# Kernel tuning notes

Measured on AMD Instinct MI355X. Metric: run time of the kernel, lower is better.

The kernel has to match this reference:

```python
import jax, jax.numpy as jnp
import numpy as np

TOP_K = 8
NUM_GROUPS = 8


def setup_inputs() -> dict:
    key = jax.random.key(0)
    ks = jax.random.split(key, 6)
    T_B, T_S, H, I, E, G = 1, 2048, 2048, 768, 32, NUM_GROUPS
    hidden_states = jax.random.normal(ks[0], (T_B, T_S, H), dtype=jnp.float32)
    gate_weight = jax.random.normal(ks[1], (E, H), dtype=jnp.float32) * 0.02
    gate_up_proj = jax.random.normal(ks[2], (E, 2 * I, H), dtype=jnp.float32) * 0.02
    down_proj = jax.random.normal(ks[3], (E, H, I), dtype=jnp.float32) * 0.02
    merge_groups = jax.random.randint(ks[4], (E,), 0, G, dtype=jnp.int64)
    # ensure every group id appears at least once so dominant experts are well-defined
    merge_groups = merge_groups.at[:G].set(jnp.arange(G, dtype=jnp.int64))
    dominant_experts = jax.random.randint(ks[5], (G,), 0, E, dtype=jnp.int64)
    return {
        "hidden_states": hidden_states,
        "gate_weight": gate_weight,
        "gate_up_proj": gate_up_proj,
        "down_proj": down_proj,
        "merge_groups": merge_groups,
        "dominant_experts": dominant_experts,
    }


def reference(hidden_states, gate_weight, gate_up_proj, down_proj, merge_groups, dominant_experts):
    B, S, H = hidden_states.shape
    G = dominant_experts.shape[0]
    x = hidden_states.reshape(-1, H)  # [T, H]

    # Router: softmax over all experts, then top-k of the probabilities (as in source)
    logits = jnp.einsum("th,eh->te", x, gate_weight)
    probs = jax.nn.softmax(logits.astype(jnp.float32), axis=-1).astype(logits.dtype)
    top_val, top_idx = jax.lax.top_k(probs, TOP_K)  # [T, K]
    top_val = top_val / jnp.sum(top_val, axis=-1, keepdims=True)  # norm_topk_prob

    # Each selected expert e is replaced by its group's dominant expert; by linearity
    # of the scatter-add combine, sum routing weights per (token, group).
    sel_group = merge_groups[top_idx]  # [T, K] in [0, G)
    onehot = jax.nn.one_hot(sel_group, G, dtype=top_val.dtype)  # [T, K, G]
    w_tg = jnp.einsum("tk,tkg->tg", top_val, onehot)  # combined weight per token/group

    gu = gate_up_proj[dominant_experts]  # [G, 2I, H]
    dn = down_proj[dominant_experts]     # [G, H, I]

    h = jnp.einsum("th,goh->tgo", x, gu)           # [T, G, 2I]
    gate, up = jnp.split(h, 2, axis=-1)              # [T, G, I] each
    act = jax.nn.silu(gate) * up                     # SwiGLU
    y = jnp.einsum("tgi,ghi->tgh", act, dn)        # [T, G, H]
    out = jnp.einsum("tg,tgh->th", w_tg, y)        # combine
    return out.reshape(B, S, H)
```

## Files before the change

### kernel.cpp

```cpp
#include <hip/hip_runtime.h>
#include <hip/hip_bf16.h>

typedef __attribute__((ext_vector_type(8))) short short8v;
typedef __attribute__((ext_vector_type(4))) float f32x4;

#define T_TOK 2048
#define HDIM  2048
#define IDIM  768
#define NGRP  8

__device__ __forceinline__ unsigned short f2b(float f){
  unsigned u = __float_as_uint(f);
  u = u + 0x7FFFu + ((u >> 16) & 1u);
  return (unsigned short)(u >> 16);
}
__device__ __forceinline__ float b2f(unsigned short s){
  return __uint_as_float(((unsigned)s) << 16);
}

__global__ __launch_bounds__(256) void router_kernel(
    const float* __restrict__ x, const float* __restrict__ gw,
    const int* __restrict__ mg, float* __restrict__ wtg,
    unsigned short* __restrict__ xb)
{
  __shared__ float xs[4][2048];
  __shared__ float lg[4][32];
  int tid = threadIdx.x;
  int t0 = blockIdx.x * 4;

  #pragma unroll
  for (int k = 0; k < 8; k++){
    int idx = k*256 + tid;
    int tok = idx >> 9, wi = idx & 511;
    float4 v = ((const float4*)(x + (size_t)(t0 + tok)*HDIM))[wi];
    ((float4*)xs[tok])[wi] = v;
    ushort4 b; b.x=f2b(v.x); b.y=f2b(v.y); b.z=f2b(v.z); b.w=f2b(v.w);
    ((ushort4*)(xb + (size_t)(t0+tok)*HDIM))[wi] = b;
  }
  __syncthreads();

  int e = tid >> 3, ch = tid & 7;
  float s0=0.f, s1=0.f, s2=0.f, s3=0.f;
  const float4* gv = (const float4*)(gw + (size_t)e*HDIM);
  #pragma unroll 4
  for (int k = 0; k < 64; k++){
    int i4 = ch + 8*k;
    float4 b  = gv[i4];
    float4 a0 = ((const float4*)xs[0])[i4];
    float4 a1 = ((const float4*)xs[1])[i4];
    float4 a2 = ((const float4*)xs[2])[i4];
    float4 a3 = ((const float4*)xs[3])[i4];
    s0 += a0.x*b.x + a0.y*b.y + a0.z*b.z + a0.w*b.w;
    s1 += a1.x*b.x + a1.y*b.y + a1.z*b.z + a1.w*b.w;
    s2 += a2.x*b.x + a2.y*b.y + a2.z*b.z + a2.w*b.w;
    s3 += a3.x*b.x + a3.y*b.y + a3.z*b.z + a3.w*b.w;
  }
  #pragma unroll
  for (int off=1; off<8; off<<=1){
    s0 += __shfl_xor(s0, off); s1 += __shfl_xor(s1, off);
    s2 += __shfl_xor(s2, off); s3 += __shfl_xor(s3, off);
  }
  if (ch == 0){ lg[0][e]=s0; lg[1][e]=s1; lg[2][e]=s2; lg[3][e]=s3; }
  __syncthreads();

  int wv = tid >> 6, lane = tid & 63;
  float val = (lane < 32) ? lg[wv][lane] : -1e30f;
  float mx = val;
  #pragma unroll
  for (int off=16; off; off>>=1) mx = fmaxf(mx, __shfl_xor(mx, off));
  float p = (lane < 32) ? expf(val - mx) : 0.f;
  float sm = p;
  #pragma unroll
  for (int off=16; off; off>>=1) sm += __shfl_xor(sm, off);
  float v = (lane < 32) ? (p / sm) : -1.f;
  int idx = lane;
  float vals[8]; int idxs[8];
  #pragma unroll
  for (int it=0; it<8; it++){
    float bv = v; int bi = idx;
    #pragma unroll
    for (int off=32; off; off>>=1){
      float ov = __shfl_xor(bv, off); int oi = __shfl_xor(bi, off);
      if (ov > bv || (ov == bv && oi < bi)){ bv = ov; bi = oi; }
    }
    vals[it] = bv; idxs[it] = bi;
    if (lane == bi) v = -1.f;
  }
  float tot = vals[0]+vals[1]+vals[2]+vals[3]+vals[4]+vals[5]+vals[6]+vals[7];
  float racc = 0.f;
  #pragma unroll
  for (int it=0; it<8; it++){
    int grp = mg[idxs[it]];
    if (lane == grp) racc += vals[it] / tot;
  }
  if (lane < 8) wtg[(size_t)(t0+wv)*NGRP + lane] = racc;
}

__global__ __launch_bounds__(256) void convert_gu_kernel(
    const float* __restrict__ src, unsigned short* __restrict__ dst,
    const int* __restrict__ de)
{
  int g = blockIdx.z;
  int i4 = blockIdx.x*256 + threadIdx.x;
  int j  = i4 >> 9;
  int c4 = i4 & 511;
  int q = j >> 5, r = j & 31;
  int srow = (r < 16) ? (q*16 + r) : (768 + q*16 + (r - 16));
  const float4* s = (const float4*)(src + ((size_t)de[g]*1536 + srow)*HDIM);
  float4 vv = s[c4];
  ushort4 b; b.x=f2b(vv.x); b.y=f2b(vv.y); b.z=f2b(vv.z); b.w=f2b(vv.w);
  ((ushort4*)(dst + ((size_t)g*1536 + j)*HDIM))[c4] = b;
}

__global__ __launch_bounds__(256) void convert_dn_kernel(
    const float* __restrict__ src, unsigned short* __restrict__ dst,
    const int* __restrict__ de)
{
  int g = blockIdx.z;
  size_t i4 = (size_t)blockIdx.x*256 + threadIdx.x;
  const float4* s = (const float4*)(src + (size_t)de[g]*1572864);
  float4 vv = s[i4];
  ushort4 b; b.x=f2b(vv.x); b.y=f2b(vv.y); b.z=f2b(vv.z); b.w=f2b(vv.w);
  ((ushort4*)(dst + (size_t)g*1572864))[i4] = b;
}


template<int R>
__device__ __forceinline__ void stage_tile(const unsigned short* __restrict__ gsrc,
                                           int ldE, unsigned short* __restrict__ lds,
                                           int tid)
{
  #pragma unroll
  for (int j = 0; j < R/128; j++){
    int row = j*128 + (tid >> 2);
    const unsigned short* src = gsrc + (size_t)row*ldE + (tid & 3)*8;
    __builtin_amdgcn_global_load_lds(
        (const __attribute__((address_space(1))) void*)src,
        (__attribute__((address_space(3))) void*)(lds + j*4096 + (tid >> 6)*512),
        16, 0, 0);
  }
}

__device__ __forceinline__ short8v rfrag(const unsigned short* lds, int r, int s){
  return *(const short8v*)((const char*)lds + r*64 + (s << 4));
}

#define WAITV(N)  asm volatile("s_waitcnt vmcnt(" #N ")" ::: "memory")
#define TOPBAR()  do { __builtin_amdgcn_s_barrier(); __builtin_amdgcn_sched_barrier(0); } while(0)

__global__ __launch_bounds__(512, 2) void gemm1_kernel(
    const unsigned short* __restrict__ xb, const unsigned short* __restrict__ gu,
    const float* __restrict__ wtg, unsigned short* __restrict__ actb)
{
  __shared__ unsigned short Al[4][8192];
  __shared__ unsigned short Bl[4][4096];
  int tid = threadIdx.x, lane = tid & 63, w = tid >> 6;
  int wm = w >> 1, wn = w & 1;
  int fr = lane & 15, sl = lane >> 4;

  int bid = blockIdx.x;
  int xcd = bid & 7, j = bid >> 3;
  int panel = ((xcd & 1) ? 48 : 0) + (j >> 1);
  int mb = ((xcd >> 1) << 1) + (j & 1);
  int nb = panel % 12, g = panel / 12;
  int m0 = mb * 256, n0 = nb * 128;
  const unsigned short* Abase = xb + (size_t)m0 * HDIM;
  const unsigned short* Bbase = gu + ((size_t)g * 1536 + n0) * HDIM;

  f32x4 acc[4][4];
  #pragma unroll
  for (int m=0;m<4;m++){
    #pragma unroll
    for (int n=0;n<4;n++) acc[m][n] = (f32x4){0,0,0,0};
  }

  #define BODY1(t, DOSTAGE) do { \
    int buf = (t) & 3; \
    short8v av[4], bv[4]; \
    _Pragma("unroll") for (int m=0;m<4;m++) av[m] = rfrag(&Al[buf][0], wm*64 + m*16 + fr, sl); \
    _Pragma("unroll") for (int n=0;n<4;n++) bv[n] = rfrag(&Bl[buf][0], wn*64 + n*16 + fr, sl); \
    if (DOSTAGE){ int k2 = (t)+3, b2 = k2 & 3; \
      stage_tile<256>(Abase + k2*32, HDIM, &Al[b2][0], tid); \
      stage_tile<128>(Bbase + k2*32, HDIM, &Bl[b2][0], tid); } \
    _Pragma("unroll") for (int m=0;m<4;m++){ \
      _Pragma("unroll") for (int n=0;n<4;n++){ \
        acc[m][n] = __builtin_amdgcn_mfma_f32_16x16x32_bf16(av[m], bv[n], acc[m][n],0,0,0); } } \
  } while(0)

  const int NT = 64;
  stage_tile<256>(Abase,      HDIM, &Al[0][0], tid); stage_tile<128>(Bbase,      HDIM, &Bl[0][0], tid);
  stage_tile<256>(Abase + 32, HDIM, &Al[1][0], tid); stage_tile<128>(Bbase + 32, HDIM, &Bl[1][0], tid);
  stage_tile<256>(Abase + 64, HDIM, &Al[2][0], tid); stage_tile<128>(Bbase + 64, HDIM, &Bl[2][0], tid);

  for (int t = 0; t < NT-3; ++t){
    WAITV(6); TOPBAR();
    BODY1(t, 1);
  }
  WAITV(6); TOPBAR(); BODY1(NT-3, 0);
  WAITV(3); TOPBAR(); BODY1(NT-2, 0);
  WAITV(0); TOPBAR(); BODY1(NT-1, 0);
  #undef BODY1

  int r0 = (lane >> 4) * 4;
  int q0 = (n0 + wn*64) >> 5;
  #pragma unroll
  for (int m = 0; m < 4; m++){
    int trow = m0 + wm*64 + m*16 + r0;
    #pragma unroll
    for (int q = 0; q < 2; q++){
      int icol = (q0 + q)*16 + fr;
      #pragma unroll
      for (int jj = 0; jj < 4; jj++){
        int t = trow + jj;
        float wv = wtg[(size_t)t*NGRP + g];
        float gf = acc[m][2*q][jj];
        float uf = acc[m][2*q+1][jj];
        float sg = gf / (1.f + expf(-gf));
        actb[((size_t)g*T_TOK + t)*IDIM + icol] = f2b(sg * uf * wv);
      }
    }
  }
}

__global__ __launch_bounds__(512, 2) void gemm2_kernel(
    const unsigned short* __restrict__ actb, const unsigned short* __restrict__ dnb,
    float* __restrict__ part)
{
  __shared__ unsigned short Al[4][4096];
  __shared__ unsigned short Bl[4][8192];
  int tid = threadIdx.x, lane = tid & 63, w = tid >> 6;
  int wm = w >> 2, wn = w & 3;
  int fr = lane & 15, sl = lane >> 4;

  int bid = blockIdx.x;
  int xcd = bid & 7, j = bid >> 3;
  int panel = ((xcd & 1) ? 8 : 0) + (j >> 2);
  int mb = ((xcd >> 1) << 2) + (j & 3);
  int nb = panel & 7, z = panel >> 3;
  int m0 = mb * 128, n0 = nb * 256;

  f32x4 acc[4][4];
  #pragma unroll
  for (int m=0;m<4;m++){
    #pragma unroll
    for (int n=0;n<4;n++) acc[m][n] = (f32x4){0,0,0,0};
  }

  #define STAGE2(kt, b2) do { \
    int gi = (kt) / 24; int kk = ((kt) - gi*24) * 32; int gg = z*4 + gi; \
    stage_tile<128>(actb + ((size_t)gg*T_TOK + m0)*IDIM + kk, IDIM, &Al[b2][0], tid); \
    stage_tile<256>(dnb  + ((size_t)gg*HDIM + n0)*IDIM + kk, IDIM, &Bl[b2][0], tid); \
  } while(0)

  #define BODY2(t, DOSTAGE) do { \
    int buf = (t) & 3; \
    short8v av[4], bv[4]; \
    _Pragma("unroll") for (int m=0;m<4;m++) av[m] = rfrag(&Al[buf][0], wm*64 + m*16 + fr, sl); \
    _Pragma("unroll") for (int n=0;n<4;n++) bv[n] = rfrag(&Bl[buf][0], wn*64 + n*16 + fr, sl); \
    if (DOSTAGE){ int k2 = (t)+3; STAGE2(k2, k2 & 3); } \
    _Pragma("unroll") for (int m=0;m<4;m++){ \
      _Pragma("unroll") for (int n=0;n<4;n++){ \
        acc[m][n] = __builtin_amdgcn_mfma_f32_16x16x32_bf16(av[m], bv[n], acc[m][n],0,0,0); } } \
  } while(0)

  const int NT = 96;
  STAGE2(0, 0); STAGE2(1, 1); STAGE2(2, 2);

  for (int t = 0; t < NT-3; ++t){
    WAITV(6); TOPBAR();
    BODY2(t, 1);
  }
  WAITV(6); TOPBAR(); BODY2(NT-3, 0);
  WAITV(3); TOPBAR(); BODY2(NT-2, 0);
  WAITV(0); TOPBAR(); BODY2(NT-1, 0);
  #undef BODY2
  #undef STAGE2

  float* Cb = part + (size_t)z * T_TOK * HDIM;
  int r0 = (lane >> 4) * 4;
  #pragma unroll
  for (int m = 0; m < 4; m++){
    int row = m0 + wm*64 + m*16 + r0;
    #pragma unroll
    for (int n = 0; n < 4; n++){
      int cc = n0 + wn*64 + n*16 + fr;
      #pragma unroll
      for (int jj = 0; jj < 4; jj++){
        Cb[(size_t)(row + jj)*HDIM + cc] = acc[m][n][jj];
      }
    }
  }
}

__global__ __launch_bounds__(256) void reduce_kernel(
    const float* __restrict__ p, float* __restrict__ o)
{
  size_t i = ((size_t)blockIdx.x*256 + threadIdx.x)*4;
  float4 a0 = *(const float4*)(p + i);
  float4 a1 = *(const float4*)(p + 4194304 + i);
  float4 r;
  r.x = a0.x + a1.x;
  r.y = a0.y + a1.y;
  r.z = a0.z + a1.z;
  r.w = a0.w + a1.w;
  *(float4*)(o + i) = r;
}

extern "C" void kernel_launch(void* const* d_in, const int* in_sizes, int n_in,
                              void* d_out, int out_size, void* d_ws, size_t ws_size,
                              hipStream_t stream)
{
  (void)in_sizes; (void)n_in; (void)out_size; (void)ws_size;
  const float* x   = (const float*)d_in[0];
  const float* gw  = (const float*)d_in[1];
  const float* gup = (const float*)d_in[2];
  const float* dnp = (const float*)d_in[3];
  const int*   mg  = (const int*)d_in[4];
  const int*   de  = (const int*)d_in[5];
  float* out = (float*)d_out;
  char* ws = (char*)d_ws;

  float*          wtg  = (float*)(ws + 0);
  unsigned short* xb   = (unsigned short*)(ws + 65536);
  unsigned short* dnb  = (unsigned short*)(ws + 8454144);
  unsigned short* actb = (unsigned short*)(ws + 33619968);
  unsigned short* gub  = (unsigned short*)(ws + 58785792);
  float*          part = (float*)(ws + 58785792);

  router_kernel<<<512, 256, 0, stream>>>(x, gw, mg, wtg, xb);
  convert_gu_kernel<<<dim3(3072,1,8), 256, 0, stream>>>(gup, gub, de);
  convert_dn_kernel<<<dim3(1536,1,8), 256, 0, stream>>>(dnp, dnb, de);
  gemm1_kernel<<<768, 512, 0, stream>>>(xb, gub, wtg, actb);
  gemm2_kernel<<<256, 512, 0, stream>>>(actb, dnb, part);
  reduce_kernel<<<4096, 256, 0, stream>>>(part, out);
}
```

Measured before the change: 253.9 us.

## Fuse gate_up fp32-to-bf16 conversion into gemm1 B-tile loading

Removes the separate gate_up conversion kernel. gemm1 now loads fp32 gate_up rows straight from the dominant expert through registers, converts them to bf16 and writes them to LDS, using a 3-stage buffer with a restructured wait and barrier schedule. It also adds s_setprio around the MFMA blocks and an lgkmcnt pin in both GEMMs. This saves a full conversion pass and its global round trip. In exchange each gemm1 block re-reads fp32 B, twice the bytes of bf16, and spends VALU time on conversion inside the main loop.

```diff
diff --git a/kernel.cpp b/kernel.cpp
--- a/kernel.cpp
+++ b/kernel.cpp
@@ -96,22 +96,6 @@
   if (lane < 8) wtg[(size_t)(t0+wv)*NGRP + lane] = racc;
 }
 
-__global__ __launch_bounds__(256) void convert_gu_kernel(
-    const float* __restrict__ src, unsigned short* __restrict__ dst,
-    const int* __restrict__ de)
-{
-  int g = blockIdx.z;
-  int i4 = blockIdx.x*256 + threadIdx.x;
-  int j  = i4 >> 9;
-  int c4 = i4 & 511;
-  int q = j >> 5, r = j & 31;
-  int srow = (r < 16) ? (q*16 + r) : (768 + q*16 + (r - 16));
-  const float4* s = (const float4*)(src + ((size_t)de[g]*1536 + srow)*HDIM);
-  float4 vv = s[c4];
-  ushort4 b; b.x=f2b(vv.x); b.y=f2b(vv.y); b.z=f2b(vv.z); b.w=f2b(vv.w);
-  ((ushort4*)(dst + ((size_t)g*1536 + j)*HDIM))[c4] = b;
-}
-
 __global__ __launch_bounds__(256) void convert_dn_kernel(
     const float* __restrict__ src, unsigned short* __restrict__ dst,
     const int* __restrict__ de)
@@ -126,9 +110,9 @@
 
 
 template<int R>
-__device__ __forceinline__ void stage_tile(const unsigned short* __restrict__ gsrc,
-                                           int ldE, unsigned short* __restrict__ lds,
-                                           int tid)
+__device__ __forceinline__ void stage512(const unsigned short* __restrict__ gsrc,
+                                         int ldE, unsigned short* __restrict__ lds,
+                                         int tid)
 {
   #pragma unroll
   for (int j = 0; j < R/128; j++){
@@ -146,14 +130,16 @@
 }
 
 #define WAITV(N)  asm volatile("s_waitcnt vmcnt(" #N ")" ::: "memory")
-#define TOPBAR()  do { __builtin_amdgcn_s_barrier(); __builtin_amdgcn_sched_barrier(0); } while(0)
+#define PIN()     do { asm volatile("s_waitcnt lgkmcnt(0)" ::: "memory"); __builtin_amdgcn_sched_barrier(0); } while(0)
+#define ENDBAR()  do { __builtin_amdgcn_s_barrier(); __builtin_amdgcn_sched_barrier(0); } while(0)
 
 __global__ __launch_bounds__(512, 2) void gemm1_kernel(
-    const unsigned short* __restrict__ xb, const unsigned short* __restrict__ gu,
-    const float* __restrict__ wtg, unsigned short* __restrict__ actb)
-{
-  __shared__ unsigned short Al[4][8192];
-  __shared__ unsigned short Bl[4][4096];
+    const unsigned short* __restrict__ xb, const float* __restrict__ gup,
+    const int* __restrict__ de, const float* __restrict__ wtg,
+    unsigned short* __restrict__ actb)
+{
+  __shared__ unsigned short Al[3][8192];
+  __shared__ unsigned short Bl[3][4096];
   int tid = threadIdx.x, lane = tid & 63, w = tid >> 6;
   int wm = w >> 1, wn = w & 1;
   int fr = lane & 15, sl = lane >> 4;
@@ -165,7 +151,12 @@
   int nb = panel % 12, g = panel / 12;
   int m0 = mb * 256, n0 = nb * 128;
   const unsigned short* Abase = xb + (size_t)m0 * HDIM;
-  const unsigned short* Bbase = gu + ((size_t)g * 1536 + n0) * HDIM;
+
+  int Jrow = n0 + (tid >> 2);
+  int qq = Jrow >> 5, rr = Jrow & 31;
+  int srow = (rr < 16) ? (qq*16 + rr) : (768 + qq*16 + (rr - 16));
+  const float* Bsrc = gup + ((size_t)de[g]*1536 + srow)*HDIM + (tid & 3)*8;
+  int boff = (tid >> 2)*32 + (tid & 3)*8;
 
   f32x4 acc[4][4];
   #pragma unroll
@@ -173,33 +164,57 @@
     #pragma unroll
     for (int n=0;n<4;n++) acc[m][n] = (f32x4){0,0,0,0};
   }
-
-  #define BODY1(t, DOSTAGE) do { \
-    int buf = (t) & 3; \
+  float4 bA[3], bB[3];
+
+  #define PFA1(T, SB) stage512<256>(Abase + (T)*32, HDIM, &Al[SB][0], tid)
+  #define PFB1(T, SB) do { const float* bs_ = Bsrc + (T)*32; \
+    bA[SB] = *(const float4*)bs_; bB[SB] = *(const float4*)(bs_ + 4); } while(0)
+  #define WRB1(WB) do { \
+    short8v pk_; \
+    pk_[0]=(short)f2b(bA[WB].x); pk_[1]=(short)f2b(bA[WB].y); \
+    pk_[2]=(short)f2b(bA[WB].z); pk_[3]=(short)f2b(bA[WB].w); \
+    pk_[4]=(short)f2b(bB[WB].x); pk_[5]=(short)f2b(bB[WB].y); \
+    pk_[6]=(short)f2b(bB[WB].z); pk_[7]=(short)f2b(bB[WB].w); \
+    *(short8v*)(&Bl[WB][0] + boff) = pk_; \
+  } while(0)
+
+  #define BODY1(T, CB, WB, SB, DOPF, DOWR, WVN) do { \
     short8v av[4], bv[4]; \
-    _Pragma("unroll") for (int m=0;m<4;m++) av[m] = rfrag(&Al[buf][0], wm*64 + m*16 + fr, sl); \
-    _Pragma("unroll") for (int n=0;n<4;n++) bv[n] = rfrag(&Bl[buf][0], wn*64 + n*16 + fr, sl); \
-    if (DOSTAGE){ int k2 = (t)+3, b2 = k2 & 3; \
-      stage_tile<256>(Abase + k2*32, HDIM, &Al[b2][0], tid); \
-      stage_tile<128>(Bbase + k2*32, HDIM, &Bl[b2][0], tid); } \
+    _Pragma("unroll") for (int m=0;m<4;m++) av[m] = rfrag(&Al[CB][0], wm*64 + m*16 + fr, sl); \
+    _Pragma("unroll") for (int n=0;n<4;n++) bv[n] = rfrag(&Bl[CB][0], wn*64 + n*16 + fr, sl); \
+    if (DOPF){ PFA1((T)+2, SB); PFB1((T)+2, SB); } \
+    WAITV(WVN); \
+    if (DOWR){ WRB1(WB); } \
+    PIN(); \
+    __builtin_amdgcn_s_setprio(1); \
     _Pragma("unroll") for (int m=0;m<4;m++){ \
       _Pragma("unroll") for (int n=0;n<4;n++){ \
         acc[m][n] = __builtin_amdgcn_mfma_f32_16x16x32_bf16(av[m], bv[n], acc[m][n],0,0,0); } } \
+    __builtin_amdgcn_s_setprio(0); \
+    ENDBAR(); \
   } while(0)
 
-  const int NT = 64;
-  stage_tile<256>(Abase,      HDIM, &Al[0][0], tid); stage_tile<128>(Bbase,      HDIM, &Bl[0][0], tid);
-  stage_tile<256>(Abase + 32, HDIM, &Al[1][0], tid); stage_tile<128>(Bbase + 32, HDIM, &Bl[1][0], tid);
-  stage_tile<256>(Abase + 64, HDIM, &Al[2][0], tid); stage_tile<128>(Bbase + 64, HDIM, &Bl[2][0], tid);
-
-  for (int t = 0; t < NT-3; ++t){
-    WAITV(6); TOPBAR();
-    BODY1(t, 1);
-  }
-  WAITV(6); TOPBAR(); BODY1(NT-3, 0);
-  WAITV(3); TOPBAR(); BODY1(NT-2, 0);
-  WAITV(0); TOPBAR(); BODY1(NT-1, 0);
+  PFA1(0, 0); PFB1(0, 0);
+  __builtin_amdgcn_sched_barrier(0);
+  PFA1(1, 1); PFB1(1, 1);
+  WAITV(4);
+  WRB1(0);
+  asm volatile("s_waitcnt lgkmcnt(0)" ::: "memory");
+  ENDBAR();
+
+  for (int t = 0; t < 60; t += 3){
+    BODY1(t  , 0, 1, 2, 1, 1, 4);
+    BODY1(t+1, 1, 2, 0, 1, 1, 4);
+    BODY1(t+2, 2, 0, 1, 1, 1, 4);
+  }
+  BODY1(60, 0, 1, 2, 1, 1, 4);
+  BODY1(61, 1, 2, 0, 1, 1, 4);
+  BODY1(62, 2, 0, 1, 0, 1, 0);
+  BODY1(63, 0, 1, 2, 0, 0, 0);
   #undef BODY1
+  #undef PFA1
+  #undef PFB1
+  #undef WRB1
 
   int r0 = (lane >> 4) * 4;
   int q0 = (n0 + wn*64) >> 5;
@@ -248,8 +263,8 @@
 
   #define STAGE2(kt, b2) do { \
     int gi = (kt) / 24; int kk = ((kt) - gi*24) * 32; int gg = z*4 + gi; \
-    stage_tile<128>(actb + ((size_t)gg*T_TOK + m0)*IDIM + kk, IDIM, &Al[b2][0], tid); \
-    stage_tile<256>(dnb  + ((size_t)gg*HDIM + n0)*IDIM + kk, IDIM, &Bl[b2][0], tid); \
+    stage512<128>(actb + ((size_t)gg*T_TOK + m0)*IDIM + kk, IDIM, &Al[b2][0], tid); \
+    stage512<256>(dnb  + ((size_t)gg*HDIM + n0)*IDIM + kk, IDIM, &Bl[b2][0], tid); \
   } while(0)
 
   #define BODY2(t, DOSTAGE) do { \
@@ -258,21 +273,24 @@
     _Pragma("unroll") for (int m=0;m<4;m++) av[m] = rfrag(&Al[buf][0], wm*64 + m*16 + fr, sl); \
     _Pragma("unroll") for (int n=0;n<4;n++) bv[n] = rfrag(&Bl[buf][0], wn*64 + n*16 + fr, sl); \
     if (DOSTAGE){ int k2 = (t)+3; STAGE2(k2, k2 & 3); } \
+    PIN(); \
+    __builtin_amdgcn_s_setprio(1); \
     _Pragma("unroll") for (int m=0;m<4;m++){ \
       _Pragma("unroll") for (int n=0;n<4;n++){ \
         acc[m][n] = __builtin_amdgcn_mfma_f32_16x16x32_bf16(av[m], bv[n], acc[m][n],0,0,0); } } \
+    __builtin_amdgcn_s_setprio(0); \
   } while(0)
 
   const int NT = 96;
   STAGE2(0, 0); STAGE2(1, 1); STAGE2(2, 2);
 
   for (int t = 0; t < NT-3; ++t){
-    WAITV(6); TOPBAR();
+    WAITV(6); ENDBAR();
     BODY2(t, 1);
   }
-  WAITV(6); TOPBAR(); BODY2(NT-3, 0);
-  WAITV(3); TOPBAR(); BODY2(NT-2, 0);
-  WAITV(0); TOPBAR(); BODY2(NT-1, 0);
+  WAITV(6); ENDBAR(); BODY2(NT-3, 0);
+  WAITV(3); ENDBAR(); BODY2(NT-2, 0);
+  WAITV(0); ENDBAR(); BODY2(NT-1, 0);
   #undef BODY2
   #undef STAGE2
 
@@ -324,13 +342,11 @@
   unsigned short* xb   = (unsigned short*)(ws + 65536);
   unsigned short* dnb  = (unsigned short*)(ws + 8454144);
   unsigned short* actb = (unsigned short*)(ws + 33619968);
-  unsigned short* gub  = (unsigned short*)(ws + 58785792);
   float*          part = (float*)(ws + 58785792);
 
   router_kernel<<<512, 256, 0, stream>>>(x, gw, mg, wtg, xb);
-  convert_gu_kernel<<<dim3(3072,1,8), 256, 0, stream>>>(gup, gub, de);
   convert_dn_kernel<<<dim3(1536,1,8), 256, 0, stream>>>(dnp, dnb, de);
-  gemm1_kernel<<<768, 512, 0, stream>>>(xb, gub, wtg, actb);
+  gemm1_kernel<<<768, 512, 0, stream>>>(xb, gup, de, wtg, actb);
   gemm2_kernel<<<256, 512, 0, stream>>>(actb, dnb, part);
   reduce_kernel<<<4096, 256, 0, stream>>>(part, out);
 }
```

New measurement: 272.3 us. 7.2% more time.
